# Kernel optimization log

Measured on AMD Instinct MI355X. Metric: run time of the kernel, lower is better.

The kernel has to match this reference:

```python
import jax, jax.numpy as jnp
import numpy as np

INV_SQRT2 = 0.7071067811865476  # 1/sqrt(2), Haar filter coefficient

def setup_inputs() -> dict:
    key = jax.random.key(0)
    x = jax.random.normal(key, (8, 4096, 1024), dtype=jnp.float32)
    return {"x": x}

def reference(x):
    # Haar DWT along axis=1 (pywt.dwt with 'haar', even length => no padding):
    #   cA[i] = (x[2i] + x[2i+1]) / sqrt(2)
    #   cD[i] = (x[2i] - x[2i+1]) / sqrt(2)
    x_even = x[:, 0::2, :]  # [B, T/2, D]
    x_odd = x[:, 1::2, :]   # [B, T/2, D]
    cA = (x_even + x_odd) * INV_SQRT2
    cD = (x_even - x_odd) * INV_SQRT2
    return (cA, cD)
```

## Files before the change

### kernel.cpp

```cpp
#include <hip/hip_runtime.h>


#define NPAIR (8 * 2048)
#define ROWS_PER_BLOCK 4
#define NPAIR_VEC (NPAIR * 256)

typedef float f4 __attribute__((ext_vector_type(4)));

__global__ __launch_bounds__(256) void dwt_haar_kernel(
    const f4* __restrict__ x,
    f4* __restrict__ cA,
    f4* __restrict__ cD)
{
    const float k = 0.7071067811865476f;
    const int t = threadIdx.x;
    const int r0 = blockIdx.x * ROWS_PER_BLOCK;

#pragma unroll
    for (int j = 0; j < ROWS_PER_BLOCK; ++j) {
        const int r = r0 + j;
        const int e = r * 512 + t;

        const f4 a = __builtin_nontemporal_load(&x[e]);
        const f4 b = __builtin_nontemporal_load(&x[e + 256]);

        const f4 s = (a + b) * k;
        const f4 d = (a - b) * k;

        const int o = r * 256 + t;
        __builtin_nontemporal_store(s, &cA[o]);
        __builtin_nontemporal_store(d, &cD[o]);
    }
}

extern "C" void kernel_launch(void* const* d_in, const int* in_sizes, int n_in,
                              void* d_out, int out_size, void* d_ws, size_t ws_size,
                              hipStream_t stream)
{
    const f4* x = (const f4*)d_in[0];
    f4* cA = (f4*)d_out;
    f4* cD = cA + NPAIR_VEC;

    const int nblocks = NPAIR / ROWS_PER_BLOCK;
    dwt_haar_kernel<<<nblocks, 256, 0, stream>>>(x, cA, cD);
}
```

Before: 220.0 us.

## Use persistent-style grid with double-buffered register chunk loads

Replaces the many-small-blocks launch with a fixed grid of 512 blocks. Each block processes several 8-row chunks, prefetching the next chunk's loads into registers before storing the current one. The intent is to keep more memory requests in flight per thread and cut block scheduling overhead. In exchange, far fewer waves are resident per CU, so latency hiding relies on per-thread memory-level parallelism and register usage rises.

```diff
diff --git a/kernel.cpp b/kernel.cpp
--- a/kernel.cpp
+++ b/kernel.cpp
@@ -2,10 +2,30 @@
 
 
 #define NPAIR (8 * 2048)
-#define ROWS_PER_BLOCK 4
+#define CHUNK 8
+#define BLOCKS 512
+#define CHUNKS_PER_BLOCK (NPAIR / (BLOCKS * CHUNK))
 #define NPAIR_VEC (NPAIR * 256)
 
 typedef float f4 __attribute__((ext_vector_type(4)));
+
+#define LOADC(A, B, RBASE)                                             \
+    _Pragma("unroll")                                                  \
+    for (int j = 0; j < CHUNK; ++j) {                                  \
+        const int e = ((RBASE) + j) * 512 + t;                         \
+        A[j] = __builtin_nontemporal_load(&x[e]);                      \
+        B[j] = __builtin_nontemporal_load(&x[e + 256]);                \
+    }
+
+#define STOREC(A, B, RBASE)                                            \
+    _Pragma("unroll")                                                  \
+    for (int j = 0; j < CHUNK; ++j) {                                  \
+        const f4 s = (A[j] + B[j]) * k;                                \
+        const f4 d = (A[j] - B[j]) * k;                                \
+        const int o = ((RBASE) + j) * 256 + t;                         \
+        __builtin_nontemporal_store(s, &cA[o]);                        \
+        __builtin_nontemporal_store(d, &cD[o]);                        \
+    }
 
 __global__ __launch_bounds__(256) void dwt_haar_kernel(
     const f4* __restrict__ x,
@@ -14,22 +34,24 @@
 {
     const float k = 0.7071067811865476f;
     const int t = threadIdx.x;
-    const int r0 = blockIdx.x * ROWS_PER_BLOCK;
+    const int base = blockIdx.x * (CHUNK * CHUNKS_PER_BLOCK);
+
+    f4 A0[CHUNK], B0[CHUNK], A1[CHUNK], B1[CHUNK];
+
+    LOADC(A0, B0, base)
 
 #pragma unroll
-    for (int j = 0; j < ROWS_PER_BLOCK; ++j) {
-        const int r = r0 + j;
-        const int e = r * 512 + t;
+    for (int cc = 0; cc < CHUNKS_PER_BLOCK / 2; ++cc) {
+        const int c0 = 2 * cc;
+        const int c1 = 2 * cc + 1;
 
-        const f4 a = __builtin_nontemporal_load(&x[e]);
-        const f4 b = __builtin_nontemporal_load(&x[e + 256]);
+        LOADC(A1, B1, base + c1 * CHUNK)
+        STOREC(A0, B0, base + c0 * CHUNK)
 
-        const f4 s = (a + b) * k;
-        const f4 d = (a - b) * k;
-
-        const int o = r * 256 + t;
-        __builtin_nontemporal_store(s, &cA[o]);
-        __builtin_nontemporal_store(d, &cD[o]);
+        if (c1 + 1 < CHUNKS_PER_BLOCK) {
+            LOADC(A0, B0, base + (c1 + 1) * CHUNK)
+        }
+        STOREC(A1, B1, base + c1 * CHUNK)
     }
 }
 
@@ -41,6 +63,5 @@
     f4* cA = (f4*)d_out;
     f4* cD = cA + NPAIR_VEC;
 
-    const int nblocks = NPAIR / ROWS_PER_BLOCK;
-    dwt_haar_kernel<<<nblocks, 256, 0, stream>>>(x, cA, cD);
+    dwt_haar_kernel<<<BLOCKS, 256, 0, stream>>>(x, cA, cD);
 }
```

Result: no change. 221.8 us (+0.8%).
